# Kernel tuning notes

Measured on AMD Instinct MI355X. Metric: run time of the kernel, lower is better.

The kernel has to match this reference:

```python
import jax, jax.numpy as jnp
import numpy as np

EPS = 1e-5


def _bn(x, g, b):
    # BatchNorm1d in training mode: batch mean, biased variance, eps=1e-5
    m = jnp.mean(x, axis=0)
    v = jnp.var(x, axis=0)
    return (x - m) * jax.lax.rsqrt(v + EPS) * g + b


def setup_inputs() -> dict:
    key = jax.random.key(0)
    ks = jax.random.split(key, 16)
    B, N, F, H = 4096, 128, 4, 32
    w = lambda k, o, i: jax.random.normal(k, (o, i), jnp.float32) * 0.3
    d = {
        'u': jax.random.normal(ks[0], (B, N, F), jnp.float32),
        'mask': jnp.ones((B * N, 1), jnp.int32),
        # MLPphi params
        'p_bn1_g': jnp.ones((F,), jnp.float32), 'p_bn1_b': jnp.zeros((F,), jnp.float32), 'p_w1': w(ks[1], H, F),
        'p_bn2_g': jnp.ones((H,), jnp.float32), 'p_bn2_b': jnp.zeros((H,), jnp.float32), 'p_w2': w(ks[2], H, H),
        'p_bn3_g': jnp.ones((H,), jnp.float32), 'p_bn3_b': jnp.zeros((H,), jnp.float32), 'p_w3': w(ks[3], H, H),
        # MLPomega params
        'o_bn1_g': jnp.ones((F,), jnp.float32), 'o_bn1_b': jnp.zeros((F,), jnp.float32), 'o_w1': w(ks[4], H, F),
        'o_bn2_g': jnp.ones((H,), jnp.float32), 'o_bn2_b': jnp.zeros((H,), jnp.float32), 'o_w2': w(ks[5], H, H),
        'o_bn3_g': jnp.ones((H,), jnp.float32), 'o_bn3_b': jnp.zeros((H,), jnp.float32), 'o_w3': w(ks[6], H, H),
        # MLPtheta params
        't_bn1_g': jnp.ones((H,), jnp.float32), 't_bn1_b': jnp.zeros((H,), jnp.float32), 't_w1': w(ks[7], H, H),
        't_bn2_g': jnp.ones((H,), jnp.float32), 't_bn2_b': jnp.zeros((H,), jnp.float32), 't_w2': w(ks[8], H, H),
        't_bn3_g': jnp.ones((H,), jnp.float32), 't_bn3_b': jnp.zeros((H,), jnp.float32), 't_w3': w(ks[9], H, H),
        't_bn4_g': jnp.ones((H,), jnp.float32), 't_bn4_b': jnp.zeros((H,), jnp.float32),
        't_w4': w(ks[10], 1, H), 't_b4': jnp.zeros((1,), jnp.float32),
    }
    return d


def _forward(u, mask,
             p_bn1_g, p_bn1_b, p_w1, p_bn2_g, p_bn2_b, p_w2, p_bn3_g, p_bn3_b, p_w3,
             o_bn1_g, o_bn1_b, o_w1, o_bn2_g, o_bn2_b, o_w2, o_bn3_g, o_bn3_b, o_w3,
             t_bn1_g, t_bn1_b, t_w1, t_bn2_g, t_bn2_b, t_w2, t_bn3_g, t_bn3_b, t_w3,
             t_bn4_g, t_bn4_b, t_w4, t_b4):
    B, N, F = u.shape
    H = p_w1.shape[0]
    u_flat = u.reshape(-1, F)  # (B*N, F)

    # MLPphi: three BN+Linear(no bias)+Tanh blocks with residual adds (dropout=identity in eval)
    o1 = jnp.tanh(_bn(u_flat, p_bn1_g, p_bn1_b) @ p_w1.T)
    o2 = jnp.tanh(_bn(o1, p_bn2_g, p_bn2_b) @ p_w2.T)
    o3 = jnp.tanh(_bn(o1 + o2, p_bn3_g, p_bn3_b) @ p_w3.T)
    x_main = (o1 + o2 + o3).reshape(B, N, H)

    # MLPomega: BN+Linear+Tanh x2, BN+Linear, softmax over hidden dim (dim=1 of flat), then masked_fill
    a = jnp.tanh(_bn(u_flat, o_bn1_g, o_bn1_b) @ o_w1.T)
    a = jnp.tanh(_bn(a, o_bn2_g, o_bn2_b) @ o_w2.T)
    a = _bn(a, o_bn3_g, o_bn3_b) @ o_w3.T
    a = jax.nn.softmax(a, axis=1)
    a = jnp.where(mask == 0, -jnp.inf, a)
    x_attn = a.reshape(B, N, H)

    # attention pooling over neighbors
    x = jnp.sum(x_main * x_attn, axis=1)  # (B, H)

    x = jnp.tanh(_bn(x, t_bn1_g, t_bn1_b) @ t_w1.T)
    x = jnp.tanh(_bn(x, t_bn2_g, t_bn2_b) @ t_w2.T)
    x = jnp.tanh(_bn(x, t_bn3_g, t_bn3_b) @ t_w3.T)
    x = _bn(x, t_bn4_g, t_bn4_b) @ t_w4.T + t_b4
    return x


def reference(u, mask,
              p_bn1_g, p_bn1_b, p_w1, p_bn2_g, p_bn2_b, p_w2, p_bn3_g, p_bn3_b, p_w3,
              o_bn1_g, o_bn1_b, o_w1, o_bn2_g, o_bn2_b, o_w2, o_bn3_g, o_bn3_b, o_w3,
              t_bn1_g, t_bn1_b, t_w1, t_bn2_g, t_bn2_b, t_w2, t_bn3_g, t_bn3_b, t_w3,
              t_bn4_g, t_bn4_b, t_w4, t_b4):
    return _forward(u, mask,
                    p_bn1_g, p_bn1_b, p_w1, p_bn2_g, p_bn2_b, p_w2, p_bn3_g, p_bn3_b, p_w3,
                    o_bn1_g, o_bn1_b, o_w1, o_bn2_g, o_bn2_b, o_w2, o_bn3_g, o_bn3_b, o_w3,
                    t_bn1_g, t_bn1_b, t_w1, t_bn2_g, t_bn2_b, t_w2, t_bn3_g, t_bn3_b, t_w3,
                    t_bn4_g, t_bn4_b, t_w4, t_b4)
```

## Files before the change

### kernel.cpp

```cpp
#include <hip/hip_runtime.h>

typedef unsigned int u32;
typedef unsigned short u16;
typedef __attribute__((ext_vector_type(8))) _Float16 half8;
typedef __attribute__((ext_vector_type(4))) float f32x4;

#define ROWS  524288
#define BROWS 4096
#define EPS   1e-5f

#define S_U   0
#define S_O1  8
#define S_A1  72
#define S_O12 136
#define S_A2  200
#define S_X   264
#define S_X1  328
#define S_X2  392
#define S_X3  456
#define SHARD 1024
#define NSH   64

#define XSTR 40

// ... 83 lines not shown
    float* Sh = S + (blockIdx.x & (NSH-1))*SHARD;
#pragma unroll
    for (int k=0;k<4;++k){ atomicAdd(&Sh[S_U+k], s[k]); atomicAdd(&Sh[S_U+4+k], q[k]); }
  }
}
__global__ __launch_bounds__(256) void k_stats_u(const void* __restrict__ u, float* __restrict__ S){
  __shared__ int sf;
  int isf = detect_u((const u16*)u, threadIdx.x, &sf);
  if (isf) stats_u_body<true>(u,S); else stats_u_body<false>(u,S);
}

__device__ __forceinline__ void prep_u(const float* __restrict__ S, float* mr, int tid){
  if (tid < 4){
    float s=0.f, q=0.f;
    for (int sh=0; sh<NSH; ++sh){
      s += S[sh*SHARD + S_U + tid];
      q += S[sh*SHARD + S_U + 4 + tid];
    }
    float m = s*(1.0f/ROWS);
    float var = q*(1.0f/ROWS) - m*m;
    mr[tid]   = m;
    mr[4+tid] = rsqrtf(var + EPS);
  }
  __syncthreads();
}
template<bool F32>
__device__ __forceinline__ void bn_u_l(const float* mr, const void* g, const void* b,
                                       const float* f, float* xn){
#pragma unroll
  for (int k=0;k<4;++k)
    xn[k] = (f[k]-mr[k])*(rdp<F32>(g,k)*mr[4+k]) + rdp<F32>(b,k);
}

template<bool F32>
__device__ __forceinline__ void chain1_to_lds(const float* xn, const void* W1, u16* Xrow){
  u32 buf[16];
#pragma unroll
  for (int jp=0; jp<16; ++jp){
    int j0 = 2*jp, j1 = 2*jp+1;
    float a0 = tanh_fast(xn[0]*rdp<F32>(W1,j0*4+0) + xn[1]*rdp<F32>(W1,j0*4+1)
                       + xn[2]*rdp<F32>(W1,j0*4+2) + xn[3]*rdp<F32>(W1,j0*4+3));
    float a1 = tanh_fast(xn[0]*rdp<F32>(W1,j1*4+0) + xn[1]*rdp<F32>(W1,j1*4+1)
                       + xn[2]*rdp<F32>(W1,j1*4+2) + xn[3]*rdp<F32>(W1,j1*4+3));
    buf[jp] = pack2h(a0, a1);
  }
#pragma unroll
  for (int c=0;c<4;++c){
    uint4 v; v.x = buf[c*4]; v.y = buf[c*4+1]; v.z = buf[c*4+2]; v.w = buf[c*4+3];
    *(uint4*)&Xrow[c*8] = v;
  }
}

template<bool F32>
__device__ __forceinline__ void fold2(const float* __restrict__ S, int offA, int offB,
    const void* gA, const void* bA, const void* WA,
    const void* gB, const void* bB, const void* WB,
    u16* Wt, float* Cb, float* scr )
{
  int tid = threadIdx.x;
  if (tid < 64){
    int L = tid>>5, k = tid&31;
    const void* g = L? gB:gA; const void* b = L? bB:bA;
    int off = L? offB:offA;
    float s=0.f, q=0.f;
    for (int sh=0; sh<NSH; ++sh){
      s += S[sh*SHARD + off + k];
      q += S[sh*SHARD + off + 32 + k];
    }
    float m    = s*(1.0f/ROWS);
    float var  = q*(1.0f/ROWS) - m*m;
    float rstd = rsqrtf(var+EPS);
    float sc = rdp<F32>(g,k)*rstd;
    scr[tid]    = sc;
    scr[64+tid] = rdp<F32>(b,k) - m*sc;
  }
  __syncthreads();
  if (tid < 64){
    int L = tid>>5, j = tid&31;
    const void* W = L? WB:WA;
    float c = 0.f;
#pragma unroll
    for (int k=0;k<32;++k){
// ... 30 lines not shown
    f32x4 c0 = {0.f,0.f,0.f,0.f}, c1 = {0.f,0.f,0.f,0.f};
    c0 = __builtin_amdgcn_mfma_f32_16x16x32_f16(w0, bfr, c0, 0,0,0);
    c1 = __builtin_amdgcn_mfma_f32_16x16x32_f16(w1, bfr, c1, 0,0,0);
    float o0[4], o1v[4];
    if (KIND == KIND_TANHRES || KIND == KIND_TANHRES_ATREG){
      unpk4(*(const uint2*)&X[s*XSTR +      quad*4], o0);
      unpk4(*(const uint2*)&X[s*XSTR + 16 + quad*4], o1v);
    }
    float a0v[4], a1v[4];
    if (KIND == KIND_TANHRES_ATREG){
      a0v[0]=lo16(at_pk[Mt*4+0]); a0v[1]=hi16(at_pk[Mt*4+0]);
      a0v[2]=lo16(at_pk[Mt*4+1]); a0v[3]=hi16(at_pk[Mt*4+1]);
      a1v[0]=lo16(at_pk[Mt*4+2]); a1v[1]=hi16(at_pk[Mt*4+2]);
      a1v[2]=lo16(at_pk[Mt*4+3]); a1v[3]=hi16(at_pk[Mt*4+3]);
    }
    float v0[4], v1[4];
#pragma unroll
    for (int reg=0;reg<4;++reg){
      float a = c0[reg] + bias0[reg];
      float b = c1[reg] + bias1[reg];
      if (KIND == KIND_TANH){ a = tanh_fast(a); b = tanh_fast(b); }
      else if (KIND == KIND_TANHRES){ a = o0[reg] + tanh_fast(a); b = o1v[reg] + tanh_fast(b); }
      else if (KIND == KIND_TANHRES_ATREG){
        a = (o0[reg] + tanh_fast(a)) * a0v[reg];
        b = (o1v[reg] + tanh_fast(b)) * a1v[reg];
      }
      v0[reg] = a; v1[reg] = b;
    }
    uint2 w0o, w1o;
    w0o.x = pack2h(v0[0], v0[1]); w0o.y = pack2h(v0[2], v0[3]);
    w1o.x = pack2h(v1[0], v1[1]); w1o.y = pack2h(v1[2], v1[3]);
    *(uint2*)&X[s*XSTR +      quad*4] = w0o;
    *(uint2*)&X[s*XSTR + 16 + quad*4] = w1o;
  }
}

template<int KIND, bool STORE>
__device__ __forceinline__ void mfma_stat(const u16* X, const u16* Wt, const float* Cb,
    int L, int wv, int lane, u16* __restrict__ G, int gbase, float* s8, float* q8)
{
  int ln15 = lane & 15, quad = lane >> 4;
  half8 w0 = *(const half8*)&Wt[(L*32 + ln15     )*XSTR + quad*8];
  half8 w1 = *(const half8*)&Wt[(L*32 + ln15 + 16)*XSTR + quad*8];
  float bias0[4], bias1[4];
#pragma unroll
  for (int reg=0;reg<4;++reg){
    bias0[reg] = Cb[L*32 +      quad*4 + reg];
    bias1[reg] = Cb[L*32 + 16 + quad*4 + reg];
  }
#pragma unroll
  for (int i=0;i<8;++i){ s8[i]=0.f; q8[i]=0.f; }
  int rowbase = wv*64;
#pragma unroll
  for (int Mt=0; Mt<4; ++Mt){
    int s = rowbase + Mt*16 + ln15;
    half8 bfr = *(const half8*)&X[s*XSTR + quad*8];
    f32x4 c0 = {0.f,0.f,0.f,0.f}, c1 = {0.f,0.f,0.f,0.f};
    c0 = __builtin_amdgcn_mfma_f32_16x16x32_f16(w0, bfr, c0, 0,0,0);
    c1 = __builtin_amdgcn_mfma_f32_16x16x32_f16(w1, bfr, c1, 0,0,0);
    float o0[4], o1v[4];
    if (KIND == KIND_TANHRES){
      unpk4(*(const uint2*)&X[s*XSTR +      quad*4], o0);
      unpk4(*(const uint2*)&X[s*XSTR + 16 + quad*4], o1v);
    }
    float v0[4], v1[4];
#pragma unroll
    for (int reg=0;reg<4;++reg){
      float a = c0[reg] + bias0[reg];
      float b = c1[reg] + bias1[reg];
      if (KIND == KIND_TANH){ a = tanh_fast(a); b = tanh_fast(b); }
      else { a = o0[reg] + tanh_fast(a); b = o1v[reg] + tanh_fast(b); }
      s8[reg]   += a; q8[reg]   = fmaf(a,a,q8[reg]);
      s8[4+reg] += b; q8[4+reg] = fmaf(b,b,q8[4+reg]);
      v0[reg] = a; v1[reg] = b;
    }
    if (STORE){
      uint2 w0o, w1o;
      w0o.x = pack2h(v0[0], v0[1]); w0o.y = pack2h(v0[2], v0[3]);
      w1o.x = pack2h(v1[0], v1[1]); w1o.y = pack2h(v1[2], v1[3]);
      size_t R = (size_t)(gbase + s);
      *(uint2*)&G[R*32 +      quad*4] = w0o;
      *(uint2*)&G[R*32 + 16 + quad*4] = w1o;
    }
  }
}

__device__ __forceinline__ void emit_stats(float* s8, float* q8, int tid, int wv,
    int quad, int ln15, float* scr , float* __restrict__ S, int offS, int shard)
{
#pragma unroll
  for (int i=0;i<8;++i){ s8[i]=red16(s8[i]); q8[i]=red16(q8[i]); }
  __syncthreads();
  if (ln15 == 0){
#pragma unroll
    for (int rg=0; rg<4; ++rg){
      int cl = quad*4+rg, ch = 16+quad*4+rg;
      scr[wv*64 + cl]       = s8[rg];
      scr[wv*64 + ch]       = s8[4+rg];
      scr[256 + wv*64 + cl] = q8[rg];
      scr[256 + wv*64 + ch] = q8[4+rg];
    }
  }
  __syncthreads();
  if (tid < 64){
    int j = tid & 31, isq = tid >> 5;
    const float* src = scr + isq*256;
    float tot = src[j] + src[64+j] + src[128+j] + src[192+j];
    atomicAdd(&S[shard*SHARD + offS + isq*32 + j], tot);
  }
}

__device__ __forceinline__ void mfma_logits_softmax_g(const u16* __restrict__ Gsrc, int gbase,
    const u16* Wt, const float* Cb, int L, int wv, int lane,
    const int* __restrict__ mask, int maskbase, u32* at_pk)
{
  int ln15 = lane & 15, quad = lane >> 4;
// ... 108 lines not shown
    for (int sg=0;sg<8;++sg) tot += src[sg*32+j];
    atomicAdd(&S[shard*SHARD + offS + (isq?32:0) + j], tot);
  }
  __syncthreads();
}

__device__ __forceinline__ void reduce_f32(const float* Xs, float* lds2,
                                           float* __restrict__ S, int offS, int shard)
{
  int tid = threadIdx.x;
  __syncthreads();
  {
    int j = tid & 31, seg = tid >> 5;
    float s=0.f, q=0.f;
    for (int q2=0;q2<32;++q2){
      float v = Xs[(seg*32+q2)*33 + j];
      s += v; q = fmaf(v,v,q);
    }
    lds2[seg*32+j] = s;
    lds2[256 + seg*32+j] = q;
  }
  __syncthreads();
  if (tid < 64){
    int j = tid & 31; bool isq = tid >= 32;
    const float* src = lds2 + (isq?256:0);
    float tot=0.f;
#pragma unroll
    for (int sg=0;sg<8;++sg) tot += src[sg*32+j];
    atomicAdd(&S[shard*SHARD + offS + (isq?32:0) + j], tot);
  }
  __syncthreads();
}

template<bool F32>
__device__ __forceinline__ void pass1_body(const void* __restrict__ u,
    const void* pg1, const void* pb1, const void* pw1,
    const void* og1, const void* ob1, const void* ow1,
    float* __restrict__ S, u16* X, float* lds2, float* mr)
{
  int tid = threadIdx.x;
  int r = blockIdx.x*256 + tid;
  int shard = blockIdx.x & (NSH-1);
  prep_u(S, mr, tid);
  float f[4], xn[4];
  load_u4<F32>(u,r,f);

  bn_u_l<F32>(mr, pg1, pb1, f, xn);
  chain1_to_lds<F32>(xn, pw1, X + tid*XSTR);
  reduce_f16(X, lds2, S, S_O1, shard);

  bn_u_l<F32>(mr, og1, ob1, f, xn);
  chain1_to_lds<F32>(xn, ow1, X + tid*XSTR);
  reduce_f16(X, lds2, S, S_A1, shard);
}
__global__ __launch_bounds__(256) void k_pass1(const void* __restrict__ u,
    const void* pg1, const void* pb1, const void* pw1,
    const void* og1, const void* ob1, const void* ow1,
    float* __restrict__ S){
  __shared__ u16 X[256*XSTR];
  __shared__ float lds2[512];
  __shared__ float mr[8];
  __shared__ int sf;
  int isf = detect_u((const u16*)u, threadIdx.x, &sf);
  if (isf) pass1_body<true >(u,pg1,pb1,pw1,og1,ob1,ow1,S,X,lds2,mr);
  else     pass1_body<false>(u,pg1,pb1,pw1,og1,ob1,ow1,S,X,lds2,mr);
}

template<bool F32, bool MAT>
__device__ __forceinline__ void pass2_body(const void* __restrict__ u,
    const void* pg1, const void* pb1, const void* pw1,
    const void* og1, const void* ob1, const void* ow1,
    const void* pg2, const void* pb2, const void* pw2,
    const void* og2, const void* ob2, const void* ow2,
    float* __restrict__ S, u16* __restrict__ o12g, u16* __restrict__ a2g,
    u16* X, u16* Wt, float* Cb, float* lds2, float* mr)
{
  int tid = threadIdx.x;
  int wv = tid >> 6, lane = tid & 63;
  int ln15 = lane & 15, quad = lane >> 4;
  int r = blockIdx.x*256 + tid;
  int gbase = blockIdx.x*256;
  int shard = blockIdx.x & (NSH-1);
  prep_u(S, mr, tid);
  fold2<F32>(S, S_O1, S_A1, pg2,pb2,pw2, og2,ob2,ow2, Wt, Cb, lds2);

  float f[4], xn[4];
  load_u4<F32>(u,r,f);
  float s8[8], q8[8];

  bn_u_l<F32>(mr, pg1, pb1, f, xn);
  chain1_to_lds<F32>(xn, pw1, X + tid*XSTR);
  mfma_stat<KIND_TANHRES, MAT>(X, Wt, Cb, 0, wv, lane, o12g, gbase, s8, q8);
  emit_stats(s8, q8, tid, wv, quad, ln15, lds2, S, S_O12, shard);

  bn_u_l<F32>(mr, og1, ob1, f, xn);
  chain1_to_lds<F32>(xn, ow1, X + tid*XSTR);
  mfma_stat<KIND_TANH, MAT>(X, Wt, Cb, 1, wv, lane, a2g, gbase, s8, q8);
  emit_stats(s8, q8, tid, wv, quad, ln15, lds2, S, S_A2, shard);
}
template<bool MAT>
__global__ __launch_bounds__(256) void k_pass2(const void* __restrict__ u,
    const void* pg1, const void* pb1, const void* pw1,
    const void* og1, const void* ob1, const void* ow1,
    const void* pg2, const void* pb2, const void* pw2,
    const void* og2, const void* ob2, const void* ow2,
    float* __restrict__ S, u16* o12g, u16* a2g){
  __shared__ u16 X[256*XSTR];
  __shared__ u16 Wt[2*32*XSTR];
  __shared__ float Cb[64];
  __shared__ float lds2[512];
  __shared__ float mr[8];
  __shared__ int sf;
  int isf = detect_u((const u16*)u, threadIdx.x, &sf);
  if (isf) pass2_body<true ,MAT>(u,pg1,pb1,pw1,og1,ob1,ow1,pg2,pb2,pw2,og2,ob2,ow2,S,o12g,a2g,X,Wt,Cb,lds2,mr);
  else     pass2_body<false,MAT>(u,pg1,pb1,pw1,og1,ob1,ow1,pg2,pb2,pw2,og2,ob2,ow2,S,o12g,a2g,X,Wt,Cb,lds2,mr);
}

template<bool F32>
__device__ __forceinline__ void pass3m_body(const int* __restrict__ mask,
    const void* pg3, const void* pb3, const void* pw3,
    const void* og3, const void* ob3, const void* ow3,
    const u16* __restrict__ o12g, const u16* __restrict__ a2g,
    float* __restrict__ x, float* __restrict__ S,
    u16* Wt, float* Cb, float* lds2)
{
  int tid = threadIdx.x;
  int wv = tid >> 6, lane = tid & 63;
  int ln15 = lane & 15, quad = lane >> 4;
  int gbase = blockIdx.x*256;
  fold2<F32>(S, S_A2, S_O12, og3,ob3,ow3, pg3,pb3,pw3, Wt, Cb, lds2);

  u32 at_pk[16];
  int maskbase = gbase + wv*64;
  mfma_logits_softmax_g(a2g, gbase, Wt, Cb, 0, wv, lane, mask, maskbase, at_pk);

  float ps[8];
  mfma_pool_g(o12g, gbase, Wt, Cb, 1, wv, lane, at_pk, ps);

#pragma unroll
  for (int i=0;i<8;++i) ps[i]=red16(ps[i]);
  __syncthreads();
  if (ln15 == 0){
#pragma unroll
    for (int rg=0; rg<4; ++rg){
      lds2[wv*32 + quad*4+rg]    = ps[rg];
      lds2[wv*32 + 16+quad*4+rg] = ps[4+rg];
    }
  }
// ... 60 lines not shown
      Wt[(L*32+j)*XSTR + k] = f2h(Wv * scr[(L<<5)|k]);
      c += Wv * scr2[(L<<5)|k];
    }
    Cb[L*32+j] = c;
  }
  __syncthreads();
}

template<bool F32>
__device__ __forceinline__ void pass3_body(const void* __restrict__ u, const int* __restrict__ mask,
    const void* pg1, const void* pb1, const void* pw1,
    const void* og1, const void* ob1, const void* ow1,
    const void* pg2, const void* pb2, const void* pw2,
    const void* og2, const void* ob2, const void* ow2,
    const void* pg3, const void* pb3, const void* pw3,
    const void* og3, const void* ob3, const void* ow3,
    float* __restrict__ x, float* __restrict__ S,
    u16* X, u16* Wt, float* Cb, float* red2, float* mr)
{
  int tid = threadIdx.x;
  int wv = tid >> 6, lane = tid & 63;
  int r = blockIdx.x*256 + tid;
  prep_u(S, mr, tid);
  fold4<F32>(S, S_A1, S_A2, S_O1, S_O12,
             og2,ob2,ow2, og3,ob3,ow3, pg2,pb2,pw2, pg3,pb3,pw3,
             Wt, Cb, red2);

  float f[4], xn[4];
  load_u4<F32>(u,r,f);
  u32 at_pk[16];
  int maskbase = blockIdx.x*256 + wv*64;

  bn_u_l<F32>(mr, og1, ob1, f, xn);
  chain1_to_lds<F32>(xn, ow1, X + tid*XSTR);
  mfma_layer<KIND_TANH>(X, Wt, Cb, 0, wv, lane, 0);
  {
    int ln15 = lane & 15, quad = lane >> 4;
    half8 w0 = *(const half8*)&Wt[(1*32 + ln15     )*XSTR + quad*8];
    half8 w1 = *(const half8*)&Wt[(1*32 + ln15 + 16)*XSTR + quad*8];
    float bias0[4], bias1[4];
#pragma unroll
    for (int reg=0;reg<4;++reg){
      bias0[reg] = Cb[32 +      quad*4 + reg];
      bias1[reg] = Cb[32 + 16 + quad*4 + reg];
    }
    int rowbase = wv*64;
#pragma unroll
    for (int Mt=0; Mt<4; ++Mt){
      int s = rowbase + Mt*16 + ln15;
      half8 bfr = *(const half8*)&X[s*XSTR + quad*8];
      f32x4 c0 = {0.f,0.f,0.f,0.f}, c1 = {0.f,0.f,0.f,0.f};
      c0 = __builtin_amdgcn_mfma_f32_16x16x32_f16(w0, bfr, c0, 0,0,0);
      c1 = __builtin_amdgcn_mfma_f32_16x16x32_f16(w1, bfr, c1, 0,0,0);
      float l0[4], l1[4];
#pragma unroll
      for (int reg=0;reg<4;++reg){ l0[reg] = c0[reg]+bias0[reg]; l1[reg] = c1[reg]+bias1[reg]; }
      float mx = l0[0];
#pragma unroll
      for (int reg=1;reg<4;++reg) mx = fmaxf(mx, l0[reg]);
#pragma unroll
      for (int reg=0;reg<4;++reg) mx = fmaxf(mx, l1[reg]);
      mx = fmaxf(mx, __shfl_xor(mx, 16));
      mx = fmaxf(mx, __shfl_xor(mx, 32));
      float sum = 0.f;
#pragma unroll
      for (int reg=0;reg<4;++reg){ l0[reg] = __expf(l0[reg]-mx); sum += l0[reg]; }
#pragma unroll
      for (int reg=0;reg<4;++reg){ l1[reg] = __expf(l1[reg]-mx); sum += l1[reg]; }
      sum += __shfl_xor(sum, 16);
      sum += __shfl_xor(sum, 32);
      float inv = __builtin_amdgcn_rcpf(sum);
      bool mz = (mask[maskbase + Mt*16 + ln15] == 0);
#pragma unroll
      for (int reg=0;reg<4;++reg){
        l0[reg] *= inv; l1[reg] *= inv;
        if (mz){ l0[reg] = -__builtin_inff(); l1[reg] = -__builtin_inff(); }
      }
      at_pk[Mt*4+0] = pack2h(l0[0], l0[1]);
      at_pk[Mt*4+1] = pack2h(l0[2], l0[3]);
      at_pk[Mt*4+2] = pack2h(l1[0], l1[1]);
      at_pk[Mt*4+3] = pack2h(l1[2], l1[3]);
    }
  }

  bn_u_l<F32>(mr, pg1, pb1, f, xn);
  chain1_to_lds<F32>(xn, pw1, X + tid*XSTR);
  mfma_layer<KIND_TANHRES   >(X, Wt, Cb, 2, wv, lane, 0);
  mfma_layer<KIND_TANHRES_ATREG>(X, Wt, Cb, 3, wv, lane, at_pk);

  __syncthreads();
  {
    int jj = tid & 31, cgrp = (tid >> 5) & 3, half = tid >> 7;
    float s2 = 0.f;
    for (int q2=0;q2<32;++q2) s2 += h2f(X[(half*128 + cgrp*32 + q2)*XSTR + jj]);
    red2[tid] = s2;
  }
  __syncthreads();
  if (tid < 64){
    int half = tid >> 5, j = tid & 31;
    float v = red2[half*128+j] + red2[half*128+32+j] + red2[half*128+64+j] + red2[half*128+96+j];
    x[(blockIdx.x*2 + half)*32 + j] = v;
    float* Sh = S + (blockIdx.x & (NSH-1))*SHARD;
    atomicAdd(&Sh[S_X+j], v);
    atomicAdd(&Sh[S_X+32+j], v*v);
  }
}
__global__ __launch_bounds__(256) void k_pass3(const void* __restrict__ u, const int* __restrict__ mask,
    const void* pg1, const void* pb1, const void* pw1,
    const void* og1, const void* ob1, const void* ow1,
    const void* pg2, const void* pb2, const void* pw2,
    const void* og2, const void* ob2, const void* ow2,
    const void* pg3, const void* pb3, const void* pw3,
    const void* og3, const void* ob3, const void* ow3,
    float* __restrict__ x, float* __restrict__ S){
  __shared__ u16 X [256*XSTR];
  __shared__ u16 Wt[4*32*XSTR];
  __shared__ float Cb[128];
  __shared__ float red2[256];
  __shared__ float mr[8];
// ... 13 lines not shown
#pragma unroll
  for (int i = 0; i < NSH_IN/4; ++i)
    t += S[(grp + i*4)*SHARD + off + col];
  scratch[tid] = t;
  __syncthreads();
  if (tid < 64)
    scratch[tid] = scratch[tid] + scratch[64+tid] + scratch[128+tid] + scratch[192+tid];
  __syncthreads();
  if (tid < 32){
    float m   = scratch[tid]*(1.0f/BROWS);
    float var = scratch[32+tid]*(1.0f/BROWS) - m*m;
    lds2[tid]    = m;
    lds2[32+tid] = rsqrtf(var + EPS);
  }
  __syncthreads();
}

template<bool F32>
__device__ __forceinline__ void theta_layer(float* v, const float* lds2,
    const void* g, const void* b, const void* W){
  float xn[32];
#pragma unroll
  for (int k=0;k<32;++k)
    xn[k] = (v[k] - lds2[k]) * (rdp<F32>(g,k)*lds2[32+k]) + rdp<F32>(b,k);
#pragma unroll
  for (int j=0;j<32;++j){
    float acc = 0.f;
#pragma unroll
    for (int k=0;k<32;++k) acc = fmaf(rdp<F32>(W, j*32+k), xn[k], acc);
    v[j] = tanh_fast(acc);
  }
}

template<bool F32, int NSH_IN, bool FIN>
__device__ __forceinline__ void theta_L_body(const float* __restrict__ xin,
    float* __restrict__ xout, float* __restrict__ S, int off_in, int off_out,
    const void* g, const void* b, const void* W,
    const void* g4, const void* b4, const void* w4, const void* bb4,
    void* out, u32* __restrict__ ctr, int* flag,
    float* lds, float* lds2)
{
  int tid = threadIdx.x, blk = blockIdx.x;
  int r = blk*256 + tid;
  float v[32];
  {
    const float4* xr = (const float4*)&xin[(size_t)r*32];
#pragma unroll
    for (int k=0;k<8;++k){ float4 t = xr[k]; v[4*k]=t.x; v[4*k+1]=t.y; v[4*k+2]=t.z; v[4*k+3]=t.w; }
  }
  theta_gather<NSH_IN>(S, off_in, lds, lds2, tid);
  theta_layer<F32>(v, lds2, g, b, W);
  {
    float4* xw = (float4*)&xout[(size_t)r*32];
#pragma unroll
    for (int k=0;k<8;++k){ float4 t; t.x=v[4*k]; t.y=v[4*k+1]; t.z=v[4*k+2]; t.w=v[4*k+3]; xw[k]=t; }
  }
  float* Xp = lds + tid*33;
#pragma unroll
  for (int j=0;j<32;++j) Xp[j] = v[j];
  reduce_f32(lds, lds2, S, off_out, blk);

  if (FIN){
    __threadfence();
    if (tid == 0){
      u32 n = __hip_atomic_fetch_add(ctr, 1u, __ATOMIC_ACQ_REL, __HIP_MEMORY_SCOPE_AGENT);
      *flag = (n == 15);
    }
    __syncthreads();
    if (!*flag) return;
    __builtin_amdgcn_fence(__ATOMIC_ACQUIRE, "agent");
    theta_gather<16>(S, off_out, lds, lds2, tid);
#pragma unroll 1
    for (int i=0;i<16;++i){
      int r2 = i*256 + tid;
      const float4* xr = (const float4*)&xout[(size_t)r2*32];
      float acc = rdp<F32>(bb4, 0);
#pragma unroll
      for (int k8=0;k8<8;++k8){
        float4 t = xr[k8];
        float vv[4] = {t.x, t.y, t.z, t.w};
#pragma unroll
        for (int q=0;q<4;++q){
          int k = k8*4+q;
          float xnv = (vv[q] - lds2[k]) * (rdp<F32>(g4,k)*lds2[32+k]) + rdp<F32>(b4,k);
          acc = fmaf(rdp<F32>(w4,k), xnv, acc);
        }
      }
      if (F32) ((float*)out)[r2] = acc;
      else     ((u16*)out)[r2]  = f2b(acc);
    }
  }
}
template<int NSH_IN, bool FIN>
__global__ __launch_bounds__(256) void k_theta_L(const void* __restrict__ u,
    const float* __restrict__ xin, float* __restrict__ xout,
    float* __restrict__ S, int off_in, int off_out,
    const void* g, const void* b, const void* W,
    const void* g4, const void* b4, const void* w4, const void* bb4,
    void* out, u32* ctr){
  __shared__ float lds[256*33];
  __shared__ float lds2[512];
  __shared__ int sf;
  int isf = detect_u((const u16*)u, threadIdx.x, &sf);
  if (isf) theta_L_body<true , NSH_IN, FIN>(xin, xout, S, off_in, off_out, g, b, W,
                                            g4, b4, w4, bb4, out, ctr, &sf, lds, lds2);
  else     theta_L_body<false, NSH_IN, FIN>(xin, xout, S, off_in, off_out, g, b, W,
                                            g4, b4, w4, bb4, out, ctr, &sf, lds, lds2);
}

extern "C" void kernel_launch(void* const* d_in, const int* in_sizes, int n_in,
                              void* d_out, int out_size, void* d_ws, size_t ws_size,
                              hipStream_t stream)
{
  const void* u    = d_in[0];
  const int*  mask = (const int*)d_in[1];
  const void *pg1=d_in[2],  *pb1=d_in[3],  *pw1=d_in[4];
  const void *pg2=d_in[5],  *pb2=d_in[6],  *pw2=d_in[7];
  const void *pg3=d_in[8],  *pb3=d_in[9],  *pw3=d_in[10];
  const void *og1=d_in[11], *ob1=d_in[12], *ow1=d_in[13];
  const void *og2=d_in[14], *ob2=d_in[15], *ow2=d_in[16];
  const void *og3=d_in[17], *ob3=d_in[18], *ow3=d_in[19];
  const void *tg1=d_in[20], *tb1=d_in[21], *tw1=d_in[22];
  const void *tg2=d_in[23], *tb2=d_in[24], *tw2=d_in[25];
  const void *tg3=d_in[26], *tb3=d_in[27], *tw3=d_in[28];
  const void *tg4=d_in[29], *tb4=d_in[30], *tw4=d_in[31], *tbb4=d_in[32];

  char* ws = (char*)d_ws;
  u32*   ctr  = (u32*)(ws + 256);
  float* S    = (float*)(ws + 4096);
  float* x    = (float*)(ws + 524288);
  float* xb   = (float*)(ws + 1048576);

  const size_t MB = 1024*1024;
  u16* o12g = (u16*)(ws + 8*MB);
  u16* a2g  = (u16*)(ws + 40*MB);
  bool MAT = ws_size >= 73*MB;

  (void)hipMemsetAsync(ws, 0, 4096 + NSH*SHARD*4, stream);
  k_stats_u<<<1024, 256, 0, stream>>>(u, S);
  k_pass1<<<2048, 256, 0, stream>>>(u, pg1,pb1,pw1, og1,ob1,ow1, S);
  if (MAT){
    k_pass2<true ><<<2048, 256, 0, stream>>>(u, pg1,pb1,pw1, og1,ob1,ow1,
                                             pg2,pb2,pw2, og2,ob2,ow2, S, o12g, a2g);
    k_pass3m<<<2048, 256, 0, stream>>>(u, mask, pg3,pb3,pw3, og3,ob3,ow3, o12g, a2g, x, S);
  } else {
    k_pass2<false><<<2048, 256, 0, stream>>>(u, pg1,pb1,pw1, og1,ob1,ow1,
                                             pg2,pb2,pw2, og2,ob2,ow2, S, o12g, a2g);
    k_pass3<<<2048, 256, 0, stream>>>(u, mask, pg1,pb1,pw1, og1,ob1,ow1,
                                      pg2,pb2,pw2, og2,ob2,ow2,
                                      pg3,pb3,pw3, og3,ob3,ow3, x, S);
  }
  k_theta_L<64,false><<<16, 256, 0, stream>>>(u, x,  xb, S, S_X,  S_X1, tg1, tb1, tw1,
                                              nullptr,nullptr,nullptr,nullptr, nullptr, nullptr);
  k_theta_L<16,false><<<16, 256, 0, stream>>>(u, xb, x,  S, S_X1, S_X2, tg2, tb2, tw2,
                                              nullptr,nullptr,nullptr,nullptr, nullptr, nullptr);
  k_theta_L<16,true ><<<16, 256, 0, stream>>>(u, x,  xb, S, S_X2, S_X3, tg3, tb3, tw3,
                                              tg4, tb4, tw4, tbb4, d_out, ctr);
}
```

Measured before the change: 341.6 us.

## Materialize layer-1 activations in pass1 so pass2 skips recompute

In the materialized path, pass1 now writes the first-layer phi and omega activations as fp16 to global buffers. A new pass2m kernel reads them back instead of reloading u and recomputing BN plus layer 1, then overwrites the same buffers with the layer-2 outputs. Separately, the final theta BN+linear step moves out of the last theta kernel, which used an atomic counter and a single finishing block, into its own 16-block kernel. This trades extra global traffic of about 64 bytes per row for less recompute, and adds one more kernel launch.

```diff
diff --git a/kernel.cpp b/kernel.cpp
--- a/kernel.cpp
+++ b/kernel.cpp
@@ -139,8 +139,9 @@
     xn[k] = (f[k]-mr[k])*(rdp<F32>(g,k)*mr[4+k]) + rdp<F32>(b,k);
 }
 
-template<bool F32>
-__device__ __forceinline__ void chain1_to_lds(const float* xn, const void* W1, u16* Xrow){
+template<bool F32, bool STORE>
+__device__ __forceinline__ void chain1_out(const float* xn, const void* W1, u16* Xrow,
+                                           u16* __restrict__ grow){
   u32 buf[16];
 #pragma unroll
   for (int jp=0; jp<16; ++jp){
@@ -155,6 +156,7 @@
   for (int c=0;c<4;++c){
     uint4 v; v.x = buf[c*4]; v.y = buf[c*4+1]; v.z = buf[c*4+2]; v.w = buf[c*4+3];
     *(uint4*)&Xrow[c*8] = v;
+    if (STORE) *(uint4*)&grow[c*8] = v;
   }
 }
 
@@ -251,56 +253,6 @@
     w1o.x = pack2h(v1[0], v1[1]); w1o.y = pack2h(v1[2], v1[3]);
     *(uint2*)&X[s*XSTR +      quad*4] = w0o;
     *(uint2*)&X[s*XSTR + 16 + quad*4] = w1o;
-  }
-}
-
-template<int KIND, bool STORE>
-__device__ __forceinline__ void mfma_stat(const u16* X, const u16* Wt, const float* Cb,
-    int L, int wv, int lane, u16* __restrict__ G, int gbase, float* s8, float* q8)
-{
-  int ln15 = lane & 15, quad = lane >> 4;
-  half8 w0 = *(const half8*)&Wt[(L*32 + ln15     )*XSTR + quad*8];
-  half8 w1 = *(const half8*)&Wt[(L*32 + ln15 + 16)*XSTR + quad*8];
-  float bias0[4], bias1[4];
-#pragma unroll
-  for (int reg=0;reg<4;++reg){
-    bias0[reg] = Cb[L*32 +      quad*4 + reg];
-    bias1[reg] = Cb[L*32 + 16 + quad*4 + reg];
-  }
-#pragma unroll
-  for (int i=0;i<8;++i){ s8[i]=0.f; q8[i]=0.f; }
-  int rowbase = wv*64;
-#pragma unroll
-  for (int Mt=0; Mt<4; ++Mt){
-    int s = rowbase + Mt*16 + ln15;
-    half8 bfr = *(const half8*)&X[s*XSTR + quad*8];
-    f32x4 c0 = {0.f,0.f,0.f,0.f}, c1 = {0.f,0.f,0.f,0.f};
-    c0 = __builtin_amdgcn_mfma_f32_16x16x32_f16(w0, bfr, c0, 0,0,0);
-    c1 = __builtin_amdgcn_mfma_f32_16x16x32_f16(w1, bfr, c1, 0,0,0);
-    float o0[4], o1v[4];
-    if (KIND == KIND_TANHRES){
-      unpk4(*(const uint2*)&X[s*XSTR +      quad*4], o0);
-      unpk4(*(const uint2*)&X[s*XSTR + 16 + quad*4], o1v);
-    }
-    float v0[4], v1[4];
-#pragma unroll
-    for (int reg=0;reg<4;++reg){
-      float a = c0[reg] + bias0[reg];
-      float b = c1[reg] + bias1[reg];
-      if (KIND == KIND_TANH){ a = tanh_fast(a); b = tanh_fast(b); }
-      else { a = o0[reg] + tanh_fast(a); b = o1v[reg] + tanh_fast(b); }
-      s8[reg]   += a; q8[reg]   = fmaf(a,a,q8[reg]);
-      s8[4+reg] += b; q8[4+reg] = fmaf(b,b,q8[4+reg]);
-      v0[reg] = a; v1[reg] = b;
-    }
-    if (STORE){
-      uint2 w0o, w1o;
-      w0o.x = pack2h(v0[0], v0[1]); w0o.y = pack2h(v0[2], v0[3]);
-      w1o.x = pack2h(v1[0], v1[1]); w1o.y = pack2h(v1[2], v1[3]);
-      size_t R = (size_t)(gbase + s);
-      *(uint2*)&G[R*32 +      quad*4] = w0o;
-      *(uint2*)&G[R*32 + 16 + quad*4] = w1o;
-    }
   }
 }
 
@@ -475,11 +427,12 @@
   __syncthreads();
 }
 
-template<bool F32>
+template<bool F32, bool MAT>
 __device__ __forceinline__ void pass1_body(const void* __restrict__ u,
     const void* pg1, const void* pb1, const void* pw1,
     const void* og1, const void* ob1, const void* ow1,
-    float* __restrict__ S, u16* X, float* lds2, float* mr)
+    float* __restrict__ S, u16* __restrict__ o1g, u16* __restrict__ a1g,
+    u16* X, float* lds2, float* mr)
 {
   int tid = threadIdx.x;
   int r = blockIdx.x*256 + tid;
@@ -489,40 +442,192 @@
   load_u4<F32>(u,r,f);
 
   bn_u_l<F32>(mr, pg1, pb1, f, xn);
-  chain1_to_lds<F32>(xn, pw1, X + tid*XSTR);
+  chain1_out<F32,MAT>(xn, pw1, X + tid*XSTR, o1g + (size_t)r*32);
   reduce_f16(X, lds2, S, S_O1, shard);
 
   bn_u_l<F32>(mr, og1, ob1, f, xn);
-  chain1_to_lds<F32>(xn, ow1, X + tid*XSTR);
+  chain1_out<F32,MAT>(xn, ow1, X + tid*XSTR, a1g + (size_t)r*32);
   reduce_f16(X, lds2, S, S_A1, shard);
 }
+template<bool MAT>
 __global__ __launch_bounds__(256) void k_pass1(const void* __restrict__ u,
     const void* pg1, const void* pb1, const void* pw1,
     const void* og1, const void* ob1, const void* ow1,
-    float* __restrict__ S){
+    float* __restrict__ S, u16* o1g, u16* a1g){
   __shared__ u16 X[256*XSTR];
   __shared__ float lds2[512];
   __shared__ float mr[8];
   __shared__ int sf;
   int isf = detect_u((const u16*)u, threadIdx.x, &sf);
-  if (isf) pass1_body<true >(u,pg1,pb1,pw1,og1,ob1,ow1,S,X,lds2,mr);
-  else     pass1_body<false>(u,pg1,pb1,pw1,og1,ob1,ow1,S,X,lds2,mr);
-}
-
-template<bool F32, bool MAT>
+  if (isf) pass1_body<true ,MAT>(u,pg1,pb1,pw1,og1,ob1,ow1,S,o1g,a1g,X,lds2,mr);
+  else     pass1_body<false,MAT>(u,pg1,pb1,pw1,og1,ob1,ow1,S,o1g,a1g,X,lds2,mr);
+}
+
+template<bool F32>
+__device__ __forceinline__ void pass2m_body(
+    const void* pg2, const void* pb2, const void* pw2,
+    const void* og2, const void* ob2, const void* ow2,
+    float* __restrict__ S, u16* __restrict__ o12g, u16* __restrict__ a2g,
+    u16* Wt, float* Cb, float* lds2)
+{
+  int tid = threadIdx.x;
+  int wv = tid >> 6, lane = tid & 63;
+  int ln15 = lane & 15, quad = lane >> 4;
+  int gbase = blockIdx.x*256;
+  int shard = blockIdx.x & (NSH-1);
+  fold2<F32>(S, S_O1, S_A1, pg2,pb2,pw2, og2,ob2,ow2, Wt, Cb, lds2);
+
+  half8 fo[4], fa[4]; uint2 r0[4], r1[4];
+  int rowbase = wv*64;
+#pragma unroll
+  for (int Mt=0; Mt<4; ++Mt){
+    size_t R = (size_t)(gbase + rowbase + Mt*16 + ln15);
+    fo[Mt] = *(const half8*)&o12g[R*32 + quad*8];
+    r0[Mt] = *(const uint2*)&o12g[R*32 +      quad*4];
+    r1[Mt] = *(const uint2*)&o12g[R*32 + 16 + quad*4];
+    fa[Mt] = *(const half8*)&a2g [R*32 + quad*8];
+  }
+  __syncthreads();
+
+  float s8[8], q8[8];
+
+  {
+    half8 w0 = *(const half8*)&Wt[(ln15     )*XSTR + quad*8];
+    half8 w1 = *(const half8*)&Wt[(ln15 + 16)*XSTR + quad*8];
+    float bias0[4], bias1[4];
+#pragma unroll
+    for (int reg=0;reg<4;++reg){
+      bias0[reg] = Cb[     quad*4 + reg];
+      bias1[reg] = Cb[16 + quad*4 + reg];
+    }
+#pragma unroll
+    for (int i=0;i<8;++i){ s8[i]=0.f; q8[i]=0.f; }
+#pragma unroll
+    for (int Mt=0; Mt<4; ++Mt){
+      f32x4 c0 = {0.f,0.f,0.f,0.f}, c1 = {0.f,0.f,0.f,0.f};
+      c0 = __builtin_amdgcn_mfma_f32_16x16x32_f16(w0, fo[Mt], c0, 0,0,0);
+      c1 = __builtin_amdgcn_mfma_f32_16x16x32_f16(w1, fo[Mt], c1, 0,0,0);
+      float o0[4], o1v[4];
+      unpk4(r0[Mt], o0); unpk4(r1[Mt], o1v);
+      float v0[4], v1[4];
+#pragma unroll
+      for (int reg=0;reg<4;++reg){
+        float a = o0[reg]  + tanh_fast(c0[reg] + bias0[reg]);
+        float b = o1v[reg] + tanh_fast(c1[reg] + bias1[reg]);
+        s8[reg]   += a; q8[reg]   = fmaf(a,a,q8[reg]);
+        s8[4+reg] += b; q8[4+reg] = fmaf(b,b,q8[4+reg]);
+        v0[reg] = a; v1[reg] = b;
+      }
+      uint2 w0o, w1o;
+      w0o.x = pack2h(v0[0], v0[1]); w0o.y = pack2h(v0[2], v0[3]);
+      w1o.x = pack2h(v1[0], v1[1]); w1o.y = pack2h(v1[2], v1[3]);
+      size_t R = (size_t)(gbase + rowbase + Mt*16 + ln15);
+      *(uint2*)&o12g[R*32 +      quad*4] = w0o;
+      *(uint2*)&o12g[R*32 + 16 + quad*4] = w1o;
+    }
+    emit_stats(s8, q8, tid, wv, quad, ln15, lds2, S, S_O12, shard);
+  }
+
+  {
+    half8 w0 = *(const half8*)&Wt[(32 + ln15     )*XSTR + quad*8];
+    half8 w1 = *(const half8*)&Wt[(32 + ln15 + 16)*XSTR + quad*8];
+    float bias0[4], bias1[4];
+#pragma unroll
+    for (int reg=0;reg<4;++reg){
+      bias0[reg] = Cb[32 +      quad*4 + reg];
+      bias1[reg] = Cb[32 + 16 + quad*4 + reg];
+    }
+#pragma unroll
+    for (int i=0;i<8;++i){ s8[i]=0.f; q8[i]=0.f; }
+#pragma unroll
+    for (int Mt=0; Mt<4; ++Mt){
+      f32x4 c0 = {0.f,0.f,0.f,0.f}, c1 = {0.f,0.f,0.f,0.f};
+      c0 = __builtin_amdgcn_mfma_f32_16x16x32_f16(w0, fa[Mt], c0, 0,0,0);
+      c1 = __builtin_amdgcn_mfma_f32_16x16x32_f16(w1, fa[Mt], c1, 0,0,0);
+      float v0[4], v1[4];
+#pragma unroll
+      for (int reg=0;reg<4;++reg){
+        float a = tanh_fast(c0[reg] + bias0[reg]);
+        float b = tanh_fast(c1[reg] + bias1[reg]);
+        s8[reg]   += a; q8[reg]   = fmaf(a,a,q8[reg]);
+        s8[4+reg] += b; q8[4+reg] = fmaf(b,b,q8[4+reg]);
+        v0[reg] = a; v1[reg] = b;
+      }
+      uint2 w0o, w1o;
+      w0o.x = pack2h(v0[0], v0[1]); w0o.y = pack2h(v0[2], v0[3]);
+      w1o.x = pack2h(v1[0], v1[1]); w1o.y = pack2h(v1[2], v1[3]);
+      size_t R = (size_t)(gbase + rowbase + Mt*16 + ln15);
+      *(uint2*)&a2g[R*32 +      quad*4] = w0o;
+      *(uint2*)&a2g[R*32 + 16 + quad*4] = w1o;
+    }
+    emit_stats(s8, q8, tid, wv, quad, ln15, lds2, S, S_A2, shard);
+  }
+}
+__global__ __launch_bounds__(256) void k_pass2m(const void* __restrict__ u,
+    const void* pg2, const void* pb2, const void* pw2,
+    const void* og2, const void* ob2, const void* ow2,
+    float* __restrict__ S, u16* o12g, u16* a2g){
+  __shared__ u16 Wt[2*32*XSTR];
+  __shared__ float Cb[64];
+  __shared__ float lds2[512];
+  __shared__ int sf;
+  int isf = detect_u((const u16*)u, threadIdx.x, &sf);
+  if (isf) pass2m_body<true >(pg2,pb2,pw2,og2,ob2,ow2,S,o12g,a2g,Wt,Cb,lds2);
+  else     pass2m_body<false>(pg2,pb2,pw2,og2,ob2,ow2,S,o12g,a2g,Wt,Cb,lds2);
+}
+
+template<int KIND>
+__device__ __forceinline__ void mfma_stat_l(const u16* X, const u16* Wt, const float* Cb,
+    int L, int wv, int lane, float* s8, float* q8)
+{
+  int ln15 = lane & 15, quad = lane >> 4;
+  half8 w0 = *(const half8*)&Wt[(L*32 + ln15     )*XSTR + quad*8];
+  half8 w1 = *(const half8*)&Wt[(L*32 + ln15 + 16)*XSTR + quad*8];
+  float bias0[4], bias1[4];
+#pragma unroll
+  for (int reg=0;reg<4;++reg){
+    bias0[reg] = Cb[L*32 +      quad*4 + reg];
+    bias1[reg] = Cb[L*32 + 16 + quad*4 + reg];
+  }
+#pragma unroll
+  for (int i=0;i<8;++i){ s8[i]=0.f; q8[i]=0.f; }
+  int rowbase = wv*64;
+#pragma unroll
+  for (int Mt=0; Mt<4; ++Mt){
+    int s = rowbase + Mt*16 + ln15;
+    half8 bfr = *(const half8*)&X[s*XSTR + quad*8];
+    f32x4 c0 = {0.f,0.f,0.f,0.f}, c1 = {0.f,0.f,0.f,0.f};
+    c0 = __builtin_amdgcn_mfma_f32_16x16x32_f16(w0, bfr, c0, 0,0,0);
+    c1 = __builtin_amdgcn_mfma_f32_16x16x32_f16(w1, bfr, c1, 0,0,0);
+    float o0[4], o1v[4];
+    if (KIND == KIND_TANHRES){
+      unpk4(*(const uint2*)&X[s*XSTR +      quad*4], o0);
+      unpk4(*(const uint2*)&X[s*XSTR + 16 + quad*4], o1v);
+    }
+#pragma unroll
+    for (int reg=0;reg<4;++reg){
+      float a = c0[reg] + bias0[reg];
+      float b = c1[reg] + bias1[reg];
+      if (KIND == KIND_TANH){ a = tanh_fast(a); b = tanh_fast(b); }
+      else { a = o0[reg] + tanh_fast(a); b = o1v[reg] + tanh_fast(b); }
+      s8[reg]   += a; q8[reg]   = fmaf(a,a,q8[reg]);
+      s8[4+reg] += b; q8[4+reg] = fmaf(b,b,q8[4+reg]);
+    }
+  }
+}
+template<bool F32>
 __device__ __forceinline__ void pass2_body(const void* __restrict__ u,
     const void* pg1, const void* pb1, const void* pw1,
     const void* og1, const void* ob1, const void* ow1,
     const void* pg2, const void* pb2, const void* pw2,
     const void* og2, const void* ob2, const void* ow2,
-    float* __restrict__ S, u16* __restrict__ o12g, u16* __restrict__ a2g,
+    float* __restrict__ S,
     u16* X, u16* Wt, float* Cb, float* lds2, float* mr)
 {
   int tid = threadIdx.x;
   int wv = tid >> 6, lane = tid & 63;
   int ln15 = lane & 15, quad = lane >> 4;
   int r = blockIdx.x*256 + tid;
-  int gbase = blockIdx.x*256;
   int shard = blockIdx.x & (NSH-1);
   prep_u(S, mr, tid);
   fold2<F32>(S, S_O1, S_A1, pg2,pb2,pw2, og2,ob2,ow2, Wt, Cb, lds2);
@@ -532,22 +637,23 @@
   float s8[8], q8[8];
 
   bn_u_l<F32>(mr, pg1, pb1, f, xn);
-  chain1_to_lds<F32>(xn, pw1, X + tid*XSTR);
-  mfma_stat<KIND_TANHRES, MAT>(X, Wt, Cb, 0, wv, lane, o12g, gbase, s8, q8);
+  chain1_out<F32,false>(xn, pw1, X + tid*XSTR, 0);
+  __syncthreads();
+  mfma_stat_l<KIND_TANHRES>(X, Wt, Cb, 0, wv, lane, s8, q8);
   emit_stats(s8, q8, tid, wv, quad, ln15, lds2, S, S_O12, shard);
 
   bn_u_l<F32>(mr, og1, ob1, f, xn);
-  chain1_to_lds<F32>(xn, ow1, X + tid*XSTR);
-  mfma_stat<KIND_TANH, MAT>(X, Wt, Cb, 1, wv, lane, a2g, gbase, s8, q8);
+  chain1_out<F32,false>(xn, ow1, X + tid*XSTR, 0);
+  __syncthreads();
+  mfma_stat_l<KIND_TANH>(X, Wt, Cb, 1, wv, lane, s8, q8);
   emit_stats(s8, q8, tid, wv, quad, ln15, lds2, S, S_A2, shard);
 }
-template<bool MAT>
 __global__ __launch_bounds__(256) void k_pass2(const void* __restrict__ u,
     const void* pg1, const void* pb1, const void* pw1,
     const void* og1, const void* ob1, const void* ow1,
     const void* pg2, const void* pb2, const void* pw2,
     const void* og2, const void* ob2, const void* ow2,
-    float* __restrict__ S, u16* o12g, u16* a2g){
+    float* __restrict__ S){
   __shared__ u16 X[256*XSTR];
   __shared__ u16 Wt[2*32*XSTR];
   __shared__ float Cb[64];
@@ -555,8 +661,8 @@
   __shared__ float mr[8];
   __shared__ int sf;
   int isf = detect_u((const u16*)u, threadIdx.x, &sf);
-  if (isf) pass2_body<true ,MAT>(u,pg1,pb1,pw1,og1,ob1,ow1,pg2,pb2,pw2,og2,ob2,ow2,S,o12g,a2g,X,Wt,Cb,lds2,mr);
-  else     pass2_body<false,MAT>(u,pg1,pb1,pw1,og1,ob1,ow1,pg2,pb2,pw2,og2,ob2,ow2,S,o12g,a2g,X,Wt,Cb,lds2,mr);
+  if (isf) pass2_body<true >(u,pg1,pb1,pw1,og1,ob1,ow1,pg2,pb2,pw2,og2,ob2,ow2,S,X,Wt,Cb,lds2,mr);
+  else     pass2_body<false>(u,pg1,pb1,pw1,og1,ob1,ow1,pg2,pb2,pw2,og2,ob2,ow2,S,X,Wt,Cb,lds2,mr);
 }
 
 template<bool F32>
@@ -683,7 +789,7 @@
   int maskbase = blockIdx.x*256 + wv*64;
 
   bn_u_l<F32>(mr, og1, ob1, f, xn);
-  chain1_to_lds<F32>(xn, ow1, X + tid*XSTR);
+  chain1_out<F32,false>(xn, ow1, X + tid*XSTR, 0);
   mfma_layer<KIND_TANH>(X, Wt, Cb, 0, wv, lane, 0);
   {
     int ln15 = lane & 15, quad = lane >> 4;
@@ -735,7 +841,7 @@
   }
 
   bn_u_l<F32>(mr, pg1, pb1, f, xn);
-  chain1_to_lds<F32>(xn, pw1, X + tid*XSTR);
+  chain1_out<F32,false>(xn, pw1, X + tid*XSTR, 0);
   mfma_layer<KIND_TANHRES   >(X, Wt, Cb, 2, wv, lane, 0);
   mfma_layer<KIND_TANHRES_ATREG>(X, Wt, Cb, 3, wv, lane, at_pk);
 
@@ -815,13 +921,10 @@
   }
 }
 
-template<bool F32, int NSH_IN, bool FIN>
+template<bool F32, int NSH_IN>
 __device__ __forceinline__ void theta_L_body(const float* __restrict__ xin,
     float* __restrict__ xout, float* __restrict__ S, int off_in, int off_out,
-    const void* g, const void* b, const void* W,
-    const void* g4, const void* b4, const void* w4, const void* bb4,
-    void* out, u32* __restrict__ ctr, int* flag,
-    float* lds, float* lds2)
+    const void* g, const void* b, const void* W, float* lds, float* lds2)
 {
   int tid = threadIdx.x, blk = blockIdx.x;
   int r = blk*256 + tid;
@@ -842,53 +945,60 @@
 #pragma unroll
   for (int j=0;j<32;++j) Xp[j] = v[j];
   reduce_f32(lds, lds2, S, off_out, blk);
-
-  if (FIN){
-    __threadfence();
-    if (tid == 0){
-      u32 n = __hip_atomic_fetch_add(ctr, 1u, __ATOMIC_ACQ_REL, __HIP_MEMORY_SCOPE_AGENT);
-      *flag = (n == 15);
-    }
-    __syncthreads();
-    if (!*flag) return;
-    __builtin_amdgcn_fence(__ATOMIC_ACQUIRE, "agent");
-    theta_gather<16>(S, off_out, lds, lds2, tid);
-#pragma unroll 1
-    for (int i=0;i<16;++i){
-      int r2 = i*256 + tid;
-      const float4* xr = (const float4*)&xout[(size_t)r2*32];
-      float acc = rdp<F32>(bb4, 0);
-#pragma unroll
-      for (int k8=0;k8<8;++k8){
-        float4 t = xr[k8];
-        float vv[4] = {t.x, t.y, t.z, t.w};
-#pragma unroll
-        for (int q=0;q<4;++q){
-          int k = k8*4+q;
-          float xnv = (vv[q] - lds2[k]) * (rdp<F32>(g4,k)*lds2[32+k]) + rdp<F32>(b4,k);
-          acc = fmaf(rdp<F32>(w4,k), xnv, acc);
-        }
-      }
-      if (F32) ((float*)out)[r2] = acc;
-      else     ((u16*)out)[r2]  = f2b(acc);
-    }
-  }
-}
-template<int NSH_IN, bool FIN>
+}
+template<int NSH_IN>
 __global__ __launch_bounds__(256) void k_theta_L(const void* __restrict__ u,
     const float* __restrict__ xin, float* __restrict__ xout,
     float* __restrict__ S, int off_in, int off_out,
-    const void* g, const void* b, const void* W,
-    const void* g4, const void* b4, const void* w4, const void* bb4,
-    void* out, u32* ctr){
+    const void* g, const void* b, const void* W){
   __shared__ float lds[256*33];
   __shared__ float lds2[512];
   __shared__ int sf;
   int isf = detect_u((const u16*)u, threadIdx.x, &sf);
-  if (isf) theta_L_body<true , NSH_IN, FIN>(xin, xout, S, off_in, off_out, g, b, W,
-                                            g4, b4, w4, bb4, out, ctr, &sf, lds, lds2);
-  else     theta_L_body<false, NSH_IN, FIN>(xin, xout, S, off_in, off_out, g, b, W,
-                                            g4, b4, w4, bb4, out, ctr, &sf, lds, lds2);
+  if (isf) theta_L_body<true , NSH_IN>(xin, xout, S, off_in, off_out, g, b, W, lds, lds2);
+  else     theta_L_body<false, NSH_IN>(xin, xout, S, off_in, off_out, g, b, W, lds, lds2);
+}
+
+template<bool F32>
+__device__ __forceinline__ void theta_fin_body(const float* __restrict__ xin,
+    float* __restrict__ S,
+    const void* g4, const void* b4, const void* w4, const void* bb4,
+    void* out, float* lds, float* lds2)
+{
+  int tid = threadIdx.x, blk = blockIdx.x;
+  int r = blk*256 + tid;
+  const float4* xr = (const float4*)&xin[(size_t)r*32];
+  float4 t0 = xr[0], t1 = xr[1], t2 = xr[2], t3 = xr[3];
+  float4 t4 = xr[4], t5 = xr[5], t6 = xr[6], t7 = xr[7];
+  theta_gather<16>(S, S_X3, lds, lds2, tid);
+  float vv[32];
+  vv[0]=t0.x; vv[1]=t0.y; vv[2]=t0.z; vv[3]=t0.w;
+  vv[4]=t1.x; vv[5]=t1.y; vv[6]=t1.z; vv[7]=t1.w;
+  vv[8]=t2.x; vv[9]=t2.y; vv[10]=t2.z; vv[11]=t2.w;
+  vv[12]=t3.x; vv[13]=t3.y; vv[14]=t3.z; vv[15]=t3.w;
+  vv[16]=t4.x; vv[17]=t4.y; vv[18]=t4.z; vv[19]=t4.w;
+  vv[20]=t5.x; vv[21]=t5.y; vv[22]=t5.z; vv[23]=t5.w;
+  vv[24]=t6.x; vv[25]=t6.y; vv[26]=t6.z; vv[27]=t6.w;
+  vv[28]=t7.x; vv[29]=t7.y; vv[30]=t7.z; vv[31]=t7.w;
+  float acc = rdp<F32>(bb4, 0);
+#pragma unroll
+  for (int k=0;k<32;++k){
+    float xnv = (vv[k] - lds2[k]) * (rdp<F32>(g4,k)*lds2[32+k]) + rdp<F32>(b4,k);
+    acc = fmaf(rdp<F32>(w4,k), xnv, acc);
+  }
+  if (F32) ((float*)out)[r] = acc;
+  else     ((u16*)out)[r]  = f2b(acc);
+}
+__global__ __launch_bounds__(256) void k_theta_fin(const void* __restrict__ u,
+    const float* __restrict__ xin, float* __restrict__ S,
+    const void* g4, const void* b4, const void* w4, const void* bb4,
+    void* out){
+  __shared__ float lds[256];
+  __shared__ float lds2[512];
+  __shared__ int sf;
+  int isf = detect_u((const u16*)u, threadIdx.x, &sf);
+  if (isf) theta_fin_body<true >(xin, S, g4, b4, w4, bb4, out, lds, lds2);
+  else     theta_fin_body<false>(xin, S, g4, b4, w4, bb4, out, lds, lds2);
 }
 
 extern "C" void kernel_launch(void* const* d_in, const int* in_sizes, int n_in,
@@ -909,7 +1019,6 @@
   const void *tg4=d_in[29], *tb4=d_in[30], *tw4=d_in[31], *tbb4=d_in[32];
 
   char* ws = (char*)d_ws;
-  u32*   ctr  = (u32*)(ws + 256);
   float* S    = (float*)(ws + 4096);
   float* x    = (float*)(ws + 524288);
   float* xb   = (float*)(ws + 1048576);
@@ -921,22 +1030,20 @@
 
   (void)hipMemsetAsync(ws, 0, 4096 + NSH*SHARD*4, stream);
   k_stats_u<<<1024, 256, 0, stream>>>(u, S);
-  k_pass1<<<2048, 256, 0, stream>>>(u, pg1,pb1,pw1, og1,ob1,ow1, S);
   if (MAT){
-    k_pass2<true ><<<2048, 256, 0, stream>>>(u, pg1,pb1,pw1, og1,ob1,ow1,
-                                             pg2,pb2,pw2, og2,ob2,ow2, S, o12g, a2g);
+    k_pass1<true ><<<2048, 256, 0, stream>>>(u, pg1,pb1,pw1, og1,ob1,ow1, S, o12g, a2g);
+    k_pass2m<<<2048, 256, 0, stream>>>(u, pg2,pb2,pw2, og2,ob2,ow2, S, o12g, a2g);
     k_pass3m<<<2048, 256, 0, stream>>>(u, mask, pg3,pb3,pw3, og3,ob3,ow3, o12g, a2g, x, S);
   } else {
-    k_pass2<false><<<2048, 256, 0, stream>>>(u, pg1,pb1,pw1, og1,ob1,ow1,
-                                             pg2,pb2,pw2, og2,ob2,ow2, S, o12g, a2g);
+    k_pass1<false><<<2048, 256, 0, stream>>>(u, pg1,pb1,pw1, og1,ob1,ow1, S, o12g, a2g);
+    k_pass2<<<2048, 256, 0, stream>>>(u, pg1,pb1,pw1, og1,ob1,ow1,
+                                      pg2,pb2,pw2, og2,ob2,ow2, S);
     k_pass3<<<2048, 256, 0, stream>>>(u, mask, pg1,pb1,pw1, og1,ob1,ow1,
                                       pg2,pb2,pw2, og2,ob2,ow2,
                                       pg3,pb3,pw3, og3,ob3,ow3, x, S);
   }
-  k_theta_L<64,false><<<16, 256, 0, stream>>>(u, x,  xb, S, S_X,  S_X1, tg1, tb1, tw1,
-                                              nullptr,nullptr,nullptr,nullptr, nullptr, nullptr);
-  k_theta_L<16,false><<<16, 256, 0, stream>>>(u, xb, x,  S, S_X1, S_X2, tg2, tb2, tw2,
-                                              nullptr,nullptr,nullptr,nullptr, nullptr, nullptr);
-  k_theta_L<16,true ><<<16, 256, 0, stream>>>(u, x,  xb, S, S_X2, S_X3, tg3, tb3, tw3,
-                                              tg4, tb4, tw4, tbb4, d_out, ctr);
-}
+  k_theta_L<64><<<16, 256, 0, stream>>>(u, x,  xb, S, S_X,  S_X1, tg1, tb1, tw1);
+  k_theta_L<16><<<16, 256, 0, stream>>>(u, xb, x,  S, S_X1, S_X2, tg2, tb2, tw2);
+  k_theta_L<16><<<16, 256, 0, stream>>>(u, x,  xb, S, S_X2, S_X3, tg3, tb3, tw3);
+  k_theta_fin<<<16, 256, 0, stream>>>(u, xb, S, tg4, tb4, tw4, tbb4, d_out);
+}
```

Result: faster. 319.1 us (-6.6%).
